# Kernel optimization log

Measured on AMD Instinct MI355X. Metric: run time of the kernel, lower is better.

The kernel has to match this reference:

```python
import jax, jax.numpy as jnp
import numpy as np
from jax import lax

B, H, W, C = 8, 128, 128, 192
NUM_HEADS = 4
EPS = 1e-12  # tf.nn.l2_normalize epsilon


def _l2_normalize(x, axis=-1):
    sq = jnp.sum(x * x, axis=axis, keepdims=True)
    return x * lax.rsqrt(jnp.maximum(sq, EPS))


def setup_inputs() -> dict:
    key = jax.random.key(0)
    k1, k2, k3, k4 = jax.random.split(key, 4)
    x = jax.random.normal(k1, (B, H, W, C), dtype=jnp.float32)
    # 1x1 conv -> stored as [C, 3C] matrix
    qkv_w = jax.random.normal(k2, (C, 3 * C), dtype=jnp.float32) * 0.05
    # depthwise 3x3 conv, groups = 3C: HWIO kernel with I=1, O=3C
    dw_w = jax.random.normal(k3, (3, 3, 1, 3 * C), dtype=jnp.float32) * 0.05
    # 1x1 projection conv -> [C, C]
    proj_w = jax.random.normal(k4, (C, C), dtype=jnp.float32) * 0.05
    temperature = jnp.ones((NUM_HEADS, 1, 1), dtype=jnp.float32)
    return {"x": x, "qkv_w": qkv_w, "dw_w": dw_w, "proj_w": proj_w,
            "temperature": temperature}


def reference(x, qkv_w, dw_w, proj_w, temperature):
    b, h, w, c = x.shape
    heads = NUM_HEADS
    c_head = c // heads
    hw = h * w

    # 1x1 conv (no bias)
    qkv = jnp.einsum('bhwc,cd->bhwd', x, qkv_w)  # [b,h,w,3c]
    # depthwise 3x3 conv, SAME padding, groups = 3c
    qkv = lax.conv_general_dilated(
        qkv, dw_w, window_strides=(1, 1), padding='SAME',
        dimension_numbers=('NHWC', 'HWIO', 'NHWC'),
        feature_group_count=3 * c)

    q, k, v = jnp.split(qkv, 3, axis=-1)  # each [b,h,w,c]
    # faithful raw row-major reshape as in the TF code
    q = q.reshape(b, heads, c_head, hw)
    k = k.reshape(b, heads, c_head, hw)
    v = v.reshape(b, heads, c_head, hw)

    q = _l2_normalize(q, axis=-1)
    k = _l2_normalize(k, axis=-1)

    # channel-wise (transposed) attention: [b,heads,c_head,c_head]
    attn = jnp.einsum('bncs,bnds->bncd', q, k)
    attn = attn * temperature[None]  # temperature: [heads,1,1]
    attn = jax.nn.softmax(attn, axis=-1)

    out = jnp.einsum('bncd,bnds->bncs', attn, v)  # [b,heads,c_head,hw]
    out = out.reshape(b, h, w, c)
    out = jnp.einsum('bhwc,cd->bhwd', out, proj_w)  # 1x1 projection
    return out
```

## Files before the change

kernel.cpp:

```cpp
#include <hip/hip_runtime.h>
#include <math.h>

#define HWP 16384
#define CIN 192
#define C3  576
#define CH  48
#define NHD 4
#define NS  64
#define PBF 3145728
#define QKPAD 68

typedef unsigned short u16;
typedef __attribute__((ext_vector_type(8))) short bf16x8;
typedef __attribute__((ext_vector_type(4))) float f32x4;

__device__ __forceinline__ u16 f2bf(float f) {
  unsigned int u = __builtin_bit_cast(unsigned int, f);
  u = (u + 0x7FFFu + ((u >> 16) & 1u)) >> 16;
  return (u16)u;
}
__device__ __forceinline__ float bflo(unsigned int u) {
  return __builtin_bit_cast(float, u << 16);
}
__device__ __forceinline__ float bfhi(unsigned int u) {
  return __builtin_bit_cast(float, u & 0xFFFF0000u);
}
__device__ __forceinline__ unsigned pk2(float a, float b) {
  return (unsigned)f2bf(a) | ((unsigned)f2bf(b) << 16);
}

__global__ __launch_bounds__(256) void convert_w_k(
    const float* __restrict__ qkvW, const float* __restrict__ projW,
    u16* __restrict__ qkvWT, u16* __restrict__ projWT) {
  int idx = blockIdx.x * 256 + threadIdx.x;
  if (idx < C3 * CIN) {
    int n = idx / CIN, k = idx % CIN;
    qkvWT[idx] = f2bf(qkvW[(size_t)k * C3 + n]);
  } else {
    int i2 = idx - C3 * CIN;
    if (i2 < CIN * CIN) {
      int n = i2 / CIN, k = i2 % CIN;
      projWT[i2] = f2bf(projW[(size_t)k * CIN + n]);
    }
  }
}

template <bool A_F32, bool C_BF16>
__global__ __launch_bounds__(256) void gemm_bf16_t(
    const void* __restrict__ Av, const u16* __restrict__ BT, void* __restrict__ Cv,
    int M, int N, int K) {
  __shared__ __align__(16) u16 As[128 * 64];
  __shared__ __align__(16) u16 Bs[64 * 64];
  const int t = threadIdx.x;
  const int lane = t & 63, wave = t >> 6;
  const int nT = N >> 6;
  const int nwg = gridDim.x;
  const int bid = blockIdx.x;
  const int q = nwg >> 3, r = nwg & 7;
  const int xcd = bid & 7, idx = bid >> 3;
  const int swz = (xcd < r) ? (xcd * (q + 1) + idx)
                            : (r * (q + 1) + (xcd - r) * q + idx);
  const int m0 = (swz / nT) * 128, n0 = (swz % nT) * 64;
  const int wm = (wave >> 1) * 64, wn = (wave & 1) * 32;
  f32x4 acc[4][2];
#pragma unroll
  for (int mi = 0; mi < 4; ++mi)
#pragma unroll
    for (int ni = 0; ni < 2; ++ni) acc[mi][ni] = (f32x4){0.f, 0.f, 0.f, 0.f};

  const int lrow = lane & 15;
  const int lkb = (lane >> 4) * 16;

  for (int k0 = 0; k0 < K; k0 += 64) {
    __syncthreads();
#pragma unroll
    for (int rr = 0; rr < 4; ++rr) {
      int slot = t + rr * 256;
      int row = slot >> 3, g = (slot & 7) * 16;
      uint4 v;
      if (A_F32) {
        const float* Af = (const float*)Av;
        const float* src = &Af[(size_t)(m0 + row) * K + k0 + (slot & 7) * 8];
        float4 f0 = *(const float4*)src;
        float4 f1 = *(const float4*)(src + 4);
        v.x = pk2(f0.x, f0.y); v.y = pk2(f0.z, f0.w);
        v.z = pk2(f1.x, f1.y); v.w = pk2(f1.z, f1.w);
      } else {
        const u16* Ab = (const u16*)Av;
        v = *(const uint4*)&Ab[(size_t)(m0 + row) * K + k0 + (slot & 7) * 8];
      }
      *(uint4*)((char*)As + row * 128 + (g ^ ((row & 7) << 4))) = v;
    }
#pragma unroll
    for (int rr = 0; rr < 2; ++rr) {
      int slot = t + rr * 256;
      int row = slot >> 3, g = (slot & 7) * 16;
      uint4 v = *(const uint4*)&BT[(size_t)(n0 + row) * K + k0 + (slot & 7) * 8];
      *(uint4*)((char*)Bs + row * 128 + (g ^ ((row & 7) << 4))) = v;
    }
    __syncthreads();
#pragma unroll
    for (int ks = 0; ks < 2; ++ks) {
      bf16x8 a[4], b[2];
#pragma unroll
      for (int mi = 0; mi < 4; ++mi) {
        int row = wm + mi * 16 + lrow;
        int colb = ks * 64 + lkb;
        a[mi] = *(const bf16x8*)((char*)As + row * 128 + (colb ^ ((row & 7) << 4)));
      }
#pragma unroll
      for (int ni = 0; ni < 2; ++ni) {
        int row = wn + ni * 16 + lrow;
        int colb = ks * 64 + lkb;
        b[ni] = *(const bf16x8*)((char*)Bs + row * 128 + (colb ^ ((row & 7) << 4)));
      }
#pragma unroll
      for (int mi = 0; mi < 4; ++mi)
#pragma unroll
        for (int ni = 0; ni < 2; ++ni)
          acc[mi][ni] = __builtin_amdgcn_mfma_f32_16x16x32_bf16(a[mi], b[ni], acc[mi][ni], 0, 0, 0);
    }
  }
  const int crow = (lane >> 4) * 4, ccol = lane & 15;
#pragma unroll
  for (int mi = 0; mi < 4; ++mi)
#pragma unroll
    for (int ni = 0; ni < 2; ++ni)
#pragma unroll
      for (int rr = 0; rr < 4; ++rr) {
        size_t off = (size_t)(m0 + wm + mi * 16 + crow + rr) * N + n0 + wn + ni * 16 + ccol;
        if (C_BF16) ((u16*)Cv)[off] = f2bf(acc[mi][ni][rr]);
        else        ((float*)Cv)[off] = acc[mi][ni][rr];
      }
}

__global__ __launch_bounds__(192) void dwconv_k(
    const u16* __restrict__ pre, const float* __restrict__ dwW,
    u16* __restrict__ qb, u16* __restrict__ kb, u16* __restrict__ vb,
    float* __restrict__ psum, int b0) {
  __shared__ __align__(16) u16 lds[2400 * 8];
  const int t = threadIdx.x;
  const int tile = blockIdx.x, sel = blockIdx.y, brel = blockIdx.z;
  const int h0 = (tile >> 4) * 8, w0 = (tile & 15) * 8;
  const int cg = t % 24, tw = t / 24;
  const int c = sel * 192 + cg * 8;

  float wgt[9][8];
#pragma unroll
  for (int tap = 0; tap < 9; ++tap) {
    float4 a = *(const float4*)&dwW[(size_t)tap * C3 + c];
    float4 b = *(const float4*)&dwW[(size_t)tap * C3 + c + 4];
    wgt[tap][0] = a.x; wgt[tap][1] = a.y; wgt[tap][2] = a.z; wgt[tap][3] = a.w;
    wgt[tap][4] = b.x; wgt[tap][5] = b.y; wgt[tap][6] = b.z; wgt[tap][7] = b.w;
  }

  const u16* src = pre + (size_t)brel * HWP * C3;
#pragma unroll
  for (int r = 0; r < 13; ++r) {
    int slot = t + r * 192;
    if (slot < 2400) {
      int pix = r * 8 + tw;
      int py = pix / 10, px = pix % 10;
      int gh = h0 - 1 + py, gw = w0 - 1 + px;
      uint4 v = make_uint4(0, 0, 0, 0);
      if ((unsigned)gh < 128u && (unsigned)gw < 128u)
        v = *(const uint4*)&src[(size_t)((gh << 7) + gw) * C3 + c];
      *(uint4*)&lds[slot * 8] = v;
    }
  }
  __syncthreads();

  float ssum[8] = {};
  u16* dstb = (sel == 0 ? qb : sel == 1 ? kb : vb) + (size_t)brel * PBF;
#pragma unroll
  for (int r = 0; r < 8; ++r) {
    float acc[8] = {};
#pragma unroll
    for (int dy = 0; dy < 3; ++dy)
#pragma unroll
      for (int dx = 0; dx < 3; ++dx) {
        uint4 v = *(const uint4*)&lds[(((r + dy) * 10 + tw + dx) * 24 + cg) * 8];
        const float* wg = wgt[dy * 3 + dx];
        acc[0] += bflo(v.x) * wg[0]; acc[1] += bfhi(v.x) * wg[1];
        acc[2] += bflo(v.y) * wg[2]; acc[3] += bfhi(v.y) * wg[3];
        acc[4] += bflo(v.z) * wg[4]; acc[5] += bfhi(v.z) * wg[5];
        acc[6] += bflo(v.w) * wg[6]; acc[7] += bfhi(v.w) * wg[7];
      }
    uint4 o;
    o.x = pk2(acc[0], acc[1]); o.y = pk2(acc[2], acc[3]);
    o.z = pk2(acc[4], acc[5]); o.w = pk2(acc[6], acc[7]);
    *(uint4*)&dstb[(size_t)(((h0 + r) << 7) + w0 + tw) * CIN + cg * 8] = o;
    if (sel < 2) {
#pragma unroll
      for (int i = 0; i < 8; ++i) ssum[i] += acc[i] * acc[i];
    }
  }

  if (sel < 2) {
    __syncthreads();
    float* fl = (float*)lds;
#pragma unroll
    for (int i = 0; i < 8; ++i) fl[tw * 192 + cg * 8 + i] = ssum[i];
    __syncthreads();
    float s = 0.f;
#pragma unroll
    for (int tw2 = 0; tw2 < 8; ++tw2) s += fl[tw2 * 192 + t];
    psum[(((size_t)sel * 8 + (b0 + brel)) * 192 + t) * 256 + tile] = s;
  }
}

__global__ __launch_bounds__(192) void rownorm2_k(
    const float* __restrict__ psum, float* __restrict__ rq, float* __restrict__ rk,
    int b0) {
  int sel = blockIdx.x, brel = blockIdx.y;
  int b = b0 + brel;
  int t = threadIdx.x;
  const float* p = psum + (((size_t)sel * 8 + b) * 192 + t) * 256;
  float s = 0.f;
#pragma unroll 4
  for (int i = 0; i < 256; i += 4) {
    float4 v = *(const float4*)&p[i];
    s += v.x + v.y + v.z + v.w;
  }
  (sel ? rk : rq)[b * CIN + t] = rsqrtf(fmaxf(s, 1e-12f));
}

__global__ __launch_bounds__(256) void qk_partial_k(
    const u16* __restrict__ qbuf, const u16* __restrict__ kbuf,
    float* __restrict__ partial, int b0) {
  int sc = blockIdx.x, n = blockIdx.y, brel = blockIdx.z;
  int b = b0 + brel;
  __shared__ float qs[48][QKPAD];
  __shared__ float ks[48][QKPAD];
  const u16* qp = qbuf + (size_t)brel * PBF + (size_t)n * CH * HWP;
  const u16* kp = kbuf + (size_t)brel * PBF + (size_t)n * CH * HWP;
  int t = threadIdx.x;
  int i0 = (t >> 4) * 3, j0 = (t & 15) * 3;
  float acc[3][3] = {};
  int sBeg = sc * 256;
  for (int s0 = sBeg; s0 < sBeg + 256; s0 += 64) {
    uint2 qv[3], kv[3];
#pragma unroll
    for (int rep = 0; rep < 3; ++rep) {
      int fi = t + rep * 256;
      int row = fi >> 4;
      int sv = (fi & 15) * 4;
      qv[rep] = *(const uint2*)&qp[(size_t)row * HWP + s0 + sv];
      kv[rep] = *(const uint2*)&kp[(size_t)row * HWP + s0 + sv];
    }
    __syncthreads();
#pragma unroll
    for (int rep = 0; rep < 3; ++rep) {
      int fi = t + rep * 256;
      int row = fi >> 4;
      int sv = (fi & 15) * 4;
      qs[row][sv + 0] = bflo(qv[rep].x); qs[row][sv + 1] = bfhi(qv[rep].x);
      qs[row][sv + 2] = bflo(qv[rep].y); qs[row][sv + 3] = bfhi(qv[rep].y);
      ks[row][sv + 0] = bflo(kv[rep].x); ks[row][sv + 1] = bfhi(kv[rep].x);
      ks[row][sv + 2] = bflo(kv[rep].y); ks[row][sv + 3] = bfhi(kv[rep].y);
    }
    __syncthreads();
#pragma unroll
    for (int s4 = 0; s4 < 16; ++s4) {
      float4 q0 = *(const float4*)&qs[i0 + 0][s4 * 4];
      float4 q1 = *(const float4*)&qs[i0 + 1][s4 * 4];
      float4 q2 = *(const float4*)&qs[i0 + 2][s4 * 4];
      float4 k0 = *(const float4*)&ks[j0 + 0][s4 * 4];
      float4 k1 = *(const float4*)&ks[j0 + 1][s4 * 4];
      float4 k2 = *(const float4*)&ks[j0 + 2][s4 * 4];
      acc[0][0] += q0.x*k0.x + q0.y*k0.y + q0.z*k0.z + q0.w*k0.w;
      acc[0][1] += q0.x*k1.x + q0.y*k1.y + q0.z*k1.z + q0.w*k1.w;
      acc[0][2] += q0.x*k2.x + q0.y*k2.y + q0.z*k2.z + q0.w*k2.w;
      acc[1][0] += q1.x*k0.x + q1.y*k0.y + q1.z*k0.z + q1.w*k0.w;
      acc[1][1] += q1.x*k1.x + q1.y*k1.y + q1.z*k1.z + q1.w*k1.w;
      acc[1][2] += q1.x*k2.x + q1.y*k2.y + q1.z*k2.z + q1.w*k2.w;
      acc[2][0] += q2.x*k0.x + q2.y*k0.y + q2.z*k0.z + q2.w*k0.w;
      acc[2][1] += q2.x*k1.x + q2.y*k1.y + q2.z*k1.z + q2.w*k1.w;
      acc[2][2] += q2.x*k2.x + q2.y*k2.y + q2.z*k2.z + q2.w*k2.w;
    }
    __syncthreads();
  }
#pragma unroll
  for (int ii = 0; ii < 3; ++ii)
#pragma unroll
    for (int jj = 0; jj < 3; ++jj)
      partial[((((size_t)b * NHD + n) * NS + sc) * CH + (i0 + ii)) * CH + (j0 + jj)] = acc[ii][jj];
}

__global__ __launch_bounds__(64) void softmax_k(
    const float* __restrict__ partial, const float* __restrict__ rq, const float* __restrict__ rk,
    const float* __restrict__ temp, float* __restrict__ attn, int b0) {
  int i = blockIdx.x % CH;
  int n = (blockIdx.x / CH) % NHD;
  int brel = blockIdx.x / (CH * NHD);
  int b = b0 + brel;
  int j = threadIdx.x;
  float logit = -INFINITY;
  if (j < CH) {
    float s = 0.f;
#pragma unroll 8
    for (int sc = 0; sc < NS; ++sc)
      s += partial[((((size_t)b * NHD + n) * NS + sc) * CH + i) * CH + j];
    logit = s * rq[b * CIN + n * CH + i] * rk[b * CIN + n * CH + j] * temp[n];
  }
  float m = logit;
#pragma unroll
  for (int o = 32; o > 0; o >>= 1) m = fmaxf(m, __shfl_xor(m, o));
  float e = (j < CH) ? expf(logit - m) : 0.f;
  float sum = e;
#pragma unroll
  for (int o = 32; o > 0; o >>= 1) sum += __shfl_xor(sum, o);
  if (j < CH) attn[(((size_t)b * NHD + n) * CH + i) * CH + j] = e / sum;
}

__global__ __launch_bounds__(256) void av_k(
    const float* __restrict__ attn, const u16* __restrict__ vbuf,
    u16* __restrict__ obuf, int b0) {
  int st = blockIdx.x, n = blockIdx.y, brel = blockIdx.z;
  int b = b0 + brel;
  __shared__ float as_[CH * CH];
  int t = threadIdx.x;
  const float* ap = attn + ((size_t)b * NHD + n) * CH * CH;
#pragma unroll
  for (int r = 0; r < 9; ++r) as_[t + r * 256] = ap[t + r * 256];
  __syncthreads();
  int s = st * 512 + t * 2;
  const u16* vp = vbuf + (size_t)brel * PBF + (size_t)n * CH * HWP;
  float2 acc[CH];
#pragma unroll
  for (int d = 0; d < CH; ++d) { acc[d].x = 0.f; acc[d].y = 0.f; }
#pragma unroll 4
  for (int j4 = 0; j4 < 12; ++j4) {
    unsigned int u0 = *(const unsigned int*)&vp[(size_t)(j4 * 4 + 0) * HWP + s];
    unsigned int u1 = *(const unsigned int*)&vp[(size_t)(j4 * 4 + 1) * HWP + s];
    unsigned int u2 = *(const unsigned int*)&vp[(size_t)(j4 * 4 + 2) * HWP + s];
    unsigned int u3 = *(const unsigned int*)&vp[(size_t)(j4 * 4 + 3) * HWP + s];
    float2 v0 = make_float2(bflo(u0), bfhi(u0));
    float2 v1 = make_float2(bflo(u1), bfhi(u1));
    float2 v2 = make_float2(bflo(u2), bfhi(u2));
    float2 v3 = make_float2(bflo(u3), bfhi(u3));
#pragma unroll
    for (int d = 0; d < CH; ++d) {
      float4 a4 = *(const float4*)&as_[d * CH + j4 * 4];
      acc[d].x += a4.x * v0.x + a4.y * v1.x + a4.z * v2.x + a4.w * v3.x;
      acc[d].y += a4.x * v0.y + a4.y * v1.y + a4.z * v2.y + a4.w * v3.y;
    }
  }
  u16* op = obuf + (size_t)brel * PBF + (size_t)n * CH * HWP;
#pragma unroll
  for (int d = 0; d < CH; ++d) {
    ushort2 o; o.x = f2bf(acc[d].x); o.y = f2bf(acc[d].y);
    *(ushort2*)&op[(size_t)d * HWP + s] = o;
  }
}

extern "C" void kernel_launch(void* const* d_in, const int* in_sizes, int n_in,
                              void* d_out, int out_size, void* d_ws, size_t ws_size,
                              hipStream_t stream) {
  const float* x      = (const float*)d_in[0];
  const float* qkv_w  = (const float*)d_in[1];
  const float* dw_w   = (const float*)d_in[2];
  const float* proj_w = (const float*)d_in[3];
  const float* temp   = (const float*)d_in[4];
  float* out = (float*)d_out;

  float* rq      = (float*)d_ws;
  float* rk      = rq + 8 * CIN;
  float* attn    = rk + 8 * CIN;
  float* partial = attn + 8 * NHD * CH * CH;
  float* psum    = partial + (size_t)8 * NHD * NS * CH * CH;
  u16* qkvwT  = (u16*)(psum + (size_t)2 * 8 * 192 * 256);
  u16* projwT = qkvwT + (size_t)C3 * CIN;
  char* bufbase = (char*)(projwT + (size_t)CIN * CIN);
  size_t off = (size_t)(bufbase - (char*)d_ws);
  off = (off + 255) & ~(size_t)255;

  const size_t perBatchBytes = (size_t)HWP * C3 * 2 + 4 * (size_t)PBF * 2;
  size_t avail = ws_size > off ? ws_size - off : 0;
  int nb = (int)(avail / perBatchBytes);
  if (nb < 1) nb = 1;
  if (nb > 8) nb = 8;

  u16* qkv_pre = (u16*)((char*)d_ws + off);
  u16* qbuf = qkv_pre + (size_t)nb * HWP * C3;
  u16* kbuf = qbuf + (size_t)nb * PBF;
  u16* vbuf = kbuf + (size_t)nb * PBF;
  u16* obuf = vbuf + (size_t)nb * PBF;

  convert_w_k<<<dim3((C3 * CIN + CIN * CIN + 255) / 256), 256, 0, stream>>>(
      qkv_w, proj_w, qkvwT, projwT);

  for (int b0 = 0; b0 < 8; b0 += nb) {
    int nbc = (8 - b0) < nb ? (8 - b0) : nb;
    int M = nbc * HWP;
    gemm_bf16_t<true, true><<<dim3((M / 128) * (C3 / 64)), 256, 0, stream>>>(
        x + (size_t)b0 * HWP * CIN, qkvwT, qkv_pre, M, C3, CIN);
    dwconv_k<<<dim3(256, 3, nbc), 192, 0, stream>>>(
        qkv_pre, dw_w, qbuf, kbuf, vbuf, psum, b0);
    rownorm2_k<<<dim3(2, nbc), 192, 0, stream>>>(psum, rq, rk, b0);
    qk_partial_k<<<dim3(NS, NHD, nbc), 256, 0, stream>>>(qbuf, kbuf, partial, b0);
    softmax_k<<<dim3(nbc * NHD * CH), 64, 0, stream>>>(partial, rq, rk, temp, attn, b0);
    av_k<<<dim3(HWP / 512, NHD, nbc), 256, 0, stream>>>(attn, vbuf, obuf, b0);
    gemm_bf16_t<false, false><<<dim3((M / 128) * (CIN / 64)), 256, 0, stream>>>(
        obuf, projwT, out + (size_t)b0 * HWP * CIN, M, CIN, CIN);
  }
}
```

Measured before the change: 393.5 us.

## Replace tiled GEMM with skinny-K GEMM loading A fragments directly from global

The two 1x1-conv GEMMs (K=192) now preload the whole 64x192 B tile into LDS once and read the A operand straight from global memory into MFMA registers, removing the per-K-step A staging through LDS and the barriers inside the K loop. The K loop is fully unrolled over six 32-wide steps. The cost is uncoalesced, strided A loads per lane (each lane reads 16- or 32-byte chunks from separate rows), more register pressure, and a larger B tile in LDS. Batch-stride parameters were added but are unused (zero).

```diff
diff --git a/kernel.cpp b/kernel.cpp
--- a/kernel.cpp
+++ b/kernel.cpp
@@ -9,6 +9,7 @@
 #define NS  64
 #define PBF 3145728
 #define QKPAD 68
+#define KG  192
 
 typedef unsigned short u16;
 typedef __attribute__((ext_vector_type(8))) short bf16x8;
@@ -46,13 +47,17 @@
 }
 
 template <bool A_F32, bool C_BF16>
-__global__ __launch_bounds__(256) void gemm_bf16_t(
-    const void* __restrict__ Av, const u16* __restrict__ BT, void* __restrict__ Cv,
-    int M, int N, int K) {
-  __shared__ __align__(16) u16 As[128 * 64];
-  __shared__ __align__(16) u16 Bs[64 * 64];
+__global__ __launch_bounds__(256) void gemm_skinny(
+    const void* __restrict__ Ab, const u16* __restrict__ BTb, void* __restrict__ Cv,
+    int N, long strideA, long strideBT, long strideC) {
+  __shared__ __align__(16) u16 Bs[64 * KG];
   const int t = threadIdx.x;
   const int lane = t & 63, wave = t >> 6;
+  const int z = blockIdx.z;
+  const int esz = A_F32 ? 4 : 2;
+  const char* A = (const char*)Ab + (size_t)z * strideA * esz;
+  const u16* BT = BTb + (size_t)z * strideBT;
+
   const int nT = N >> 6;
   const int nwg = gridDim.x;
   const int bid = blockIdx.x;
@@ -62,6 +67,16 @@
                             : (r * (q + 1) + (xcd - r) * q + idx);
   const int m0 = (swz / nT) * 128, n0 = (swz % nT) * 64;
   const int wm = (wave >> 1) * 64, wn = (wave & 1) * 32;
+
+#pragma unroll
+  for (int i = 0; i < 6; ++i) {
+    int slot = t + i * 256;
+    int row = slot / 24, c = slot % 24;
+    uint4 v = *(const uint4*)&BT[(size_t)(n0 + row) * KG + c * 8];
+    *(uint4*)((char*)Bs + row * 384 + ((c * 16) ^ ((row & 7) << 4))) = v;
+  }
+  __syncthreads();
+
   f32x4 acc[4][2];
 #pragma unroll
   for (int mi = 0; mi < 4; ++mi)
@@ -69,58 +84,42 @@
     for (int ni = 0; ni < 2; ++ni) acc[mi][ni] = (f32x4){0.f, 0.f, 0.f, 0.f};
 
   const int lrow = lane & 15;
-  const int lkb = (lane >> 4) * 16;
-
-  for (int k0 = 0; k0 < K; k0 += 64) {
-    __syncthreads();
-#pragma unroll
-    for (int rr = 0; rr < 4; ++rr) {
-      int slot = t + rr * 256;
-      int row = slot >> 3, g = (slot & 7) * 16;
-      uint4 v;
+  const int lko = (lane >> 4) * 8;
+  const char* arow[4];
+#pragma unroll
+  for (int mi = 0; mi < 4; ++mi)
+    arow[mi] = A + ((size_t)(m0 + wm + mi * 16 + lrow) * KG + lko) * esz;
+
+#pragma unroll
+  for (int kk = 0; kk < 6; ++kk) {
+    bf16x8 a[4], b[2];
+#pragma unroll
+    for (int mi = 0; mi < 4; ++mi) {
       if (A_F32) {
-        const float* Af = (const float*)Av;
-        const float* src = &Af[(size_t)(m0 + row) * K + k0 + (slot & 7) * 8];
-        float4 f0 = *(const float4*)src;
-        float4 f1 = *(const float4*)(src + 4);
-        v.x = pk2(f0.x, f0.y); v.y = pk2(f0.z, f0.w);
-        v.z = pk2(f1.x, f1.y); v.w = pk2(f1.z, f1.w);
+        const float* p = (const float*)(arow[mi] + kk * 32 * 4);
+        float4 f0 = *(const float4*)p;
+        float4 f1 = *(const float4*)(p + 4);
+        uint4 u;
+        u.x = pk2(f0.x, f0.y); u.y = pk2(f0.z, f0.w);
+        u.z = pk2(f1.x, f1.y); u.w = pk2(f1.z, f1.w);
+        a[mi] = __builtin_bit_cast(bf16x8, u);
       } else {
-        const u16* Ab = (const u16*)Av;
-        v = *(const uint4*)&Ab[(size_t)(m0 + row) * K + k0 + (slot & 7) * 8];
+        a[mi] = *(const bf16x8*)(arow[mi] + kk * 32 * 2);
       }
-      *(uint4*)((char*)As + row * 128 + (g ^ ((row & 7) << 4))) = v;
-    }
-#pragma unroll
-    for (int rr = 0; rr < 2; ++rr) {
-      int slot = t + rr * 256;
-      int row = slot >> 3, g = (slot & 7) * 16;
-      uint4 v = *(const uint4*)&BT[(size_t)(n0 + row) * K + k0 + (slot & 7) * 8];
-      *(uint4*)((char*)Bs + row * 128 + (g ^ ((row & 7) << 4))) = v;
-    }
-    __syncthreads();
-#pragma unroll
-    for (int ks = 0; ks < 2; ++ks) {
-      bf16x8 a[4], b[2];
-#pragma unroll
-      for (int mi = 0; mi < 4; ++mi) {
-        int row = wm + mi * 16 + lrow;
-        int colb = ks * 64 + lkb;
-        a[mi] = *(const bf16x8*)((char*)As + row * 128 + (colb ^ ((row & 7) << 4)));
-      }
-#pragma unroll
-      for (int ni = 0; ni < 2; ++ni) {
-        int row = wn + ni * 16 + lrow;
-        int colb = ks * 64 + lkb;
-        b[ni] = *(const bf16x8*)((char*)Bs + row * 128 + (colb ^ ((row & 7) << 4)));
-      }
-#pragma unroll
-      for (int mi = 0; mi < 4; ++mi)
-#pragma unroll
-        for (int ni = 0; ni < 2; ++ni)
-          acc[mi][ni] = __builtin_amdgcn_mfma_f32_16x16x32_bf16(a[mi], b[ni], acc[mi][ni], 0, 0, 0);
-    }
-  }
+    }
+#pragma unroll
+    for (int ni = 0; ni < 2; ++ni) {
+      int row = wn + ni * 16 + lrow;
+      int colb = kk * 64 + (lane >> 4) * 16;
+      b[ni] = *(const bf16x8*)((char*)Bs + row * 384 + (colb ^ ((row & 7) << 4)));
+    }
+#pragma unroll
+    for (int mi = 0; mi < 4; ++mi)
+#pragma unroll
+      for (int ni = 0; ni < 2; ++ni)
+        acc[mi][ni] = __builtin_amdgcn_mfma_f32_16x16x32_bf16(a[mi], b[ni], acc[mi][ni], 0, 0, 0);
+  }
+
   const int crow = (lane >> 4) * 4, ccol = lane & 15;
 #pragma unroll
   for (int mi = 0; mi < 4; ++mi)
@@ -128,7 +127,8 @@
     for (int ni = 0; ni < 2; ++ni)
 #pragma unroll
       for (int rr = 0; rr < 4; ++rr) {
-        size_t off = (size_t)(m0 + wm + mi * 16 + crow + rr) * N + n0 + wn + ni * 16 + ccol;
+        size_t off = (size_t)z * strideC +
+                     (size_t)(m0 + wm + mi * 16 + crow + rr) * N + n0 + wn + ni * 16 + ccol;
         if (C_BF16) ((u16*)Cv)[off] = f2bf(acc[mi][ni][rr]);
         else        ((float*)Cv)[off] = acc[mi][ni][rr];
       }
@@ -393,15 +393,15 @@
   for (int b0 = 0; b0 < 8; b0 += nb) {
     int nbc = (8 - b0) < nb ? (8 - b0) : nb;
     int M = nbc * HWP;
-    gemm_bf16_t<true, true><<<dim3((M / 128) * (C3 / 64)), 256, 0, stream>>>(
-        x + (size_t)b0 * HWP * CIN, qkvwT, qkv_pre, M, C3, CIN);
+    gemm_skinny<true, true><<<dim3((M / 128) * (C3 / 64), 1, 1), 256, 0, stream>>>(
+        x + (size_t)b0 * HWP * CIN, qkvwT, qkv_pre, C3, 0, 0, 0);
     dwconv_k<<<dim3(256, 3, nbc), 192, 0, stream>>>(
         qkv_pre, dw_w, qbuf, kbuf, vbuf, psum, b0);
     rownorm2_k<<<dim3(2, nbc), 192, 0, stream>>>(psum, rq, rk, b0);
     qk_partial_k<<<dim3(NS, NHD, nbc), 256, 0, stream>>>(qbuf, kbuf, partial, b0);
     softmax_k<<<dim3(nbc * NHD * CH), 64, 0, stream>>>(partial, rq, rk, temp, attn, b0);
     av_k<<<dim3(HWP / 512, NHD, nbc), 256, 0, stream>>>(attn, vbuf, obuf, b0);
-    gemm_bf16_t<false, false><<<dim3((M / 128) * (CIN / 64)), 256, 0, stream>>>(
-        obuf, projwT, out + (size_t)b0 * HWP * CIN, M, CIN, CIN);
-  }
-}
+    gemm_skinny<false, false><<<dim3((M / 128) * (CIN / 64), 1, 1), 256, 0, stream>>>(
+        obuf, projwT, out + (size_t)b0 * HWP * CIN, CIN, 0, 0, 0);
+  }
+}
```

New measurement: 506.6 us. +28.7%, slower.
